# Kernel tuning notes

Measured on AMD Instinct MI355X. Metric: run time of the kernel, lower is better.

## Reference

```python
import jax, jax.numpy as jnp
import numpy as np

E = 1024   # embed_dim
H = 16     # num_heads
D = E // H # head_dim
T = 1024   # tgt_len
S = 1024   # src_len
B = 2      # batch
DELTA = 1.0
SCALE = D ** -0.5


def setup_inputs() -> dict:
    key = jax.random.key(0)
    ks = jax.random.split(key, 16)
    def lin(k, o, i):
        return jax.random.normal(k, (o, i), dtype=jnp.float32) / np.float32(np.sqrt(i))
    return {
        'query': jax.random.normal(ks[0], (T, B, E), dtype=jnp.float32),
        'key_in': jax.random.normal(ks[1], (S, B, E), dtype=jnp.float32),
        'value': jax.random.normal(ks[2], (S, B, E), dtype=jnp.float32),
        'Wq': lin(ks[3], E, E), 'bq': jnp.zeros((E,), jnp.float32),
        'Wk': lin(ks[4], E, E), 'bk': jnp.zeros((E,), jnp.float32),
        'Wv': lin(ks[5], E, E), 'bv': jnp.zeros((E,), jnp.float32),
        'Whq': lin(ks[6], E, E), 'bhq': jnp.zeros((E,), jnp.float32),
        'Whk': lin(ks[7], E, E), 'bhk': jnp.zeros((E,), jnp.float32),
        'Wwp': lin(ks[8], E, E), 'bwp': jnp.zeros((E,), jnp.float32),
        'Wvp': lin(ks[9], 1, E), 'bvp': jnp.zeros((1,), jnp.float32),
        'Wo': lin(ks[10], E, E), 'bo': jnp.zeros((E,), jnp.float32),
    }


def _heads(x, L):
    # (L, B, E) -> (B*H, L, D); E splits as (H, D) so flat index is b*H + h
    return x.reshape(L, B * H, D).transpose(1, 0, 2)


def reference(query, key_in, value, Wq, bq, Wk, bk, Wv, bv, Whq, bhq, Whk, bhk,
              Wwp, bwp, Wvp, bvp, Wo, bo):
    q = (query @ Wq.T + bq) * SCALE
    k = key_in @ Wk.T + bk
    v = value @ Wv.T + bv
    hq = query @ Whq.T + bhq
    hk = key_in @ Whk.T + bhk

    qh, hqh = _heads(q, T), _heads(hq, T)
    kh, hkh, vh = _heads(k, S), _heads(hk, S), _heads(v, S)

    # content attention logits  [B*H, T, S]
    attn = jnp.einsum('btd,bsd->bts', qh, kh)

    # Gaussian center: expected source position from hq/hk alignment
    align = jax.nn.softmax(jnp.einsum('btd,bsd->bts', hqh * SCALE, hkh), axis=-1)
    pos = jnp.arange(S, dtype=attn.dtype)          # index_mask
    mean = align @ pos                              # [B*H, T]

    # Gaussian width: per-query scalar via vp(tanh(wp(query)))
    g = (jnp.tanh(query @ Wwp.T + bwp) @ Wvp.T + bvp)[..., 0]   # (T, B)
    sigma = 1.0 + DELTA * jax.nn.sigmoid(g)                      # (T, B)
    sigma_bh = jnp.broadcast_to(sigma[:, :, None], (T, B, H)).reshape(T, B * H).T

    gauss = -((pos[None, None, :] - mean[:, :, None]) ** 2) / (
        2.0 * sigma_bh[:, :, None] ** 2)

    probs = jax.nn.softmax(attn + gauss, axis=-1)
    out = jnp.einsum('bts,bsd->btd', probs, vh)     # [B*H, T, D]
    out = out.transpose(1, 0, 2).reshape(T, B, E)
    return out @ Wo.T + bo
```

## Files before the change

### kernel.cpp

```cpp
#include <hip/hip_runtime.h>
#include <hip/hip_bf16.h>
#include <hip/hip_fp16.h>

#define T_ 1024
#define S_ 1024
#define B_ 2
#define H_ 16
#define D_ 64
#define E_ 1024
#define M_ (T_*B_)
#define SCALE_ 0.125f
#define LOG2E_ 1.4426950408889634f

typedef __attribute__((ext_vector_type(8))) short short8;
typedef __attribute__((ext_vector_type(8))) _Float16 half8;
typedef __attribute__((ext_vector_type(4))) float f32x4;

#define EXP2 __builtin_amdgcn_exp2f

__device__ __forceinline__ ushort f2bf(float x) {
  unsigned u = __float_as_uint(x);
  unsigned r = (u + 0x7fffu + ((u >> 16) & 1u)) >> 16;
  return (ushort)r;
}
__device__ __forceinline__ float bf2f(ushort h) {
  return __uint_as_float(((unsigned)h) << 16);
}
__device__ __forceinline__ ushort f2h(float x) {
  __half h = __float2half(x);
  return *(ushort*)&h;
}
__device__ __forceinline__ void gld16(const void* g, void* l) {
  __builtin_amdgcn_global_load_lds(
      (const __attribute__((address_space(1))) void*)g,
      (__attribute__((address_space(3))) void*)l, 16, 0, 0);
}
__device__ __forceinline__ unsigned cvtpk_bf16(float a, float b) {
  unsigned u;
  asm("v_cvt_pk_bf16_f32 %0, %1, %2" : "=v"(u) : "v"(a), "v"(b));
  return u;
}

#define SWZ(r, col) ((r)*64 + ((col) ^ (((r)&7)<<3)))

struct CvtDesc { const float* src; ushort* bf; ushort* h16; int n4; };
struct CvtArgs { CvtDesc d[10]; };

__global__ __launch_bounds__(256) void cvt_kernel(CvtArgs a) {
  const CvtDesc d = a.d[blockIdx.y];
  const int stride = gridDim.x * 256;
  for (int i = blockIdx.x*256 + threadIdx.x; i < d.n4; i += stride) {
    float4 v = ((const float4*)d.src)[i];
    float vals[4] = {v.x, v.y, v.z, v.w};
    if (d.bf) {
      ushort h[4];
      #pragma unroll
      for (int j = 0; j < 4; ++j) h[j] = f2bf(vals[j]);
      ((ushort4*)d.bf)[i] = make_ushort4(h[0],h[1],h[2],h[3]);
    }
    if (d.h16) {
      ushort h[4];
      #pragma unroll
      for (int j = 0; j < 4; ++j) h[j] = f2h(vals[j]);
      ((ushort4*)d.h16)[i] = make_ushort4(h[0],h[1],h[2],h[3]);
    }
  }
}

struct SegP { const ushort* A; const ushort* W; const float* bias;
              ushort* outb; float* outf; float scale; int flags; };
struct GemmArgs { SegP s[6]; };

__global__ __launch_bounds__(256) void gemm_mfma(GemmArgs args) {
  __shared__ ushort sA[128*64];
  __shared__ ushort sW[64*64];
  const int id = blockIdx.x;
  const int xcd = id & 7, loc = id >> 3;
  const int x = xcd * (gridDim.x >> 7) + (loc >> 4);
  const int y = loc & 15;
  const SegP sg = args.s[x >> 4];
  const int n0 = (x & 15) * 64;
  const int m0 = y * 128;
  const int tid = threadIdx.x, wv = tid >> 6, lane = tid & 63;
  const int c = lane & 15, g = lane >> 4;
  const int wr = wv >> 1, wc = wv & 1;
  const int lrow = lane >> 3;
  const int scol = ((lane & 7) ^ lrow) * 8;

  size_t aoff[4], woff[2];
  #pragma unroll
  for (int j = 0; j < 4; ++j) {
    int rg = wv + j*4;
    aoff[j] = (size_t)(m0 + rg*8 + lrow)*1024 + scol;
  }
  #pragma unroll
  for (int j = 0; j < 2; ++j) {
    int rg = wv + j*4;
    woff[j] = (size_t)(n0 + rg*8 + lrow)*1024 + scol;
  }

  const bool isfp16 = (sg.flags & 2) != 0;
  f32x4 acc[4][2] = {};
  for (int t = 0; t < 16; ++t) {
    const int k0 = t*64;
    #pragma unroll
    for (int j = 0; j < 4; ++j) {
      int rg = wv + j*4;
      gld16(sg.A + aoff[j] + k0, &sA[rg*512]);
    }
    #pragma unroll
    for (int j = 0; j < 2; ++j) {
      int rg = wv + j*4;
      gld16(sg.W + woff[j] + k0, &sW[rg*512]);
    }
    __syncthreads();
    #pragma unroll
    for (int ks = 0; ks < 2; ++ks) {
      short8 af[4], wf[2];
      #pragma unroll
      for (int mi = 0; mi < 4; ++mi)
        af[mi] = *(const short8*)&sA[SWZ(wr*64 + mi*16 + c, ks*32 + g*8)];
      #pragma unroll
      for (int ni = 0; ni < 2; ++ni)
        wf[ni] = *(const short8*)&sW[SWZ(wc*32 + ni*16 + c, ks*32 + g*8)];
      if (isfp16) {
        #pragma unroll
        for (int mi = 0; mi < 4; ++mi)
          #pragma unroll
          for (int ni = 0; ni < 2; ++ni)
            acc[mi][ni] = __builtin_amdgcn_mfma_f32_16x16x32_f16(
                *(half8*)&af[mi], *(half8*)&wf[ni], acc[mi][ni], 0, 0, 0);
      } else {
        #pragma unroll
        for (int mi = 0; mi < 4; ++mi)
          #pragma unroll
          for (int ni = 0; ni < 2; ++ni)
            acc[mi][ni] = __builtin_amdgcn_mfma_f32_16x16x32_bf16(
                af[mi], wf[ni], acc[mi][ni], 0, 0, 0);
      }
    }
    __syncthreads();
  }

  #pragma unroll
  for (int ni = 0; ni < 2; ++ni) {
    int col = n0 + wc*32 + ni*16 + c;
    float bias = sg.bias[col];
    #pragma unroll
    for (int mi = 0; mi < 4; ++mi) {
      #pragma unroll
      for (int r = 0; r < 4; ++r) {
        int row = m0 + wr*64 + mi*16 + 4*g + r;
        float val = (acc[mi][ni][r] + bias) * sg.scale;
        if (sg.flags & 1) val = tanhf(val);
        if (isfp16)       sg.outb[(size_t)row*1024 + col] = f2h(val);
        else if (sg.outf) sg.outf[(size_t)row*1024 + col] = val;
        else              sg.outb[(size_t)row*1024 + col] = f2bf(val);
      }
    }
  }
}

__global__ __launch_bounds__(64) void vp_sigma(const ushort* __restrict__ wp,
    const float* __restrict__ Wvp, const float* __restrict__ bvp,
    float* __restrict__ sigma) {
  const int m = blockIdx.x;
  const int lane = threadIdx.x;
  float acc = 0.f;
  #pragma unroll
  for (int it = 0; it < 2; ++it) {
    int e = lane*8 + it*512;
    short8 a = *(const short8*)&wp[(size_t)m*E_ + e];
    float4 w0 = *(const float4*)&Wvp[e];
    float4 w1 = *(const float4*)&Wvp[e+4];
    acc += bf2f((ushort)a[0])*w0.x + bf2f((ushort)a[1])*w0.y
         + bf2f((ushort)a[2])*w0.z + bf2f((ushort)a[3])*w0.w
         + bf2f((ushort)a[4])*w1.x + bf2f((ushort)a[5])*w1.y
         + bf2f((ushort)a[6])*w1.z + bf2f((ushort)a[7])*w1.w;
  }
  #pragma unroll
  for (int o = 32; o; o >>= 1) acc += __shfl_xor(acc, o);
  if (lane == 0) {
    float gg = acc + bvp[0];
    sigma[m] = 1.f + 1.f/(1.f + __expf(-gg));
  }
}

__global__ __launch_bounds__(256) void attn_mfma(
    const ushort* __restrict__ q_bf, const ushort* __restrict__ k_bf,
    const ushort* __restrict__ v_bf,
    const ushort* __restrict__ hq_h16, const ushort* __restrict__ hk_h16,
    const float* __restrict__ sigma, ushort* __restrict__ ctx) {
  __shared__ ushort sK[2][64*64];
  __shared__ ushort sV[2][64*64];
  __shared__ ushort sP[4*16*64];

  const int id = blockIdx.x;
  const int loc = id >> 3;
  const int bh = (id & 7) * 4 + (loc >> 4);
  const int b = bh >> 4, h = bh & 15;
  const int t0 = (loc & 15) * 64;
  const int tid = threadIdx.x;
  const int wv = tid >> 6, lane = tid & 63;
  const int c = lane & 15, g = lane >> 4;
  const int qbase = t0 + wv * 16;
  const size_t rowstr = (size_t)B_ * E_;
  const size_t qoff = ((size_t)(qbase + c) * B_ + b) * E_ + h * 64;

  short8 qf[2];
  half8  hqf[2];
  #pragma unroll
  for (int cs = 0; cs < 2; ++cs) {
    qf[cs]  = *(const short8*)&q_bf[qoff + cs*32 + g*8];
    hqf[cs] = *(const half8*)&hq_h16[qoff + cs*32 + g*8];
  }

  const int str0 = wv*16 + (lane >> 3);
  const int str1 = str0 + 8;
  const int chk0 = ((lane & 7) ^ (str0 & 7)) * 8;
  const int chk1 = ((lane & 7) ^ (str1 & 7)) * 8;
  const int ldsst = (wv*16) * 64;

  float den = 0.f, num = 0.f;
  {
    gld16(hk_h16 + ((size_t)str0 * B_ + b) * E_ + h*64 + chk0, &sK[0][ldsst]);
    gld16(hk_h16 + ((size_t)str1 * B_ + b) * E_ + h*64 + chk1, &sK[0][ldsst + 512]);
    __syncthreads();
    for (int t = 0; t < 16; ++t) {
      const ushort* kb = sK[t & 1];
      if (t < 15) {
        int s0n = (t+1) * 64;
        gld16(hk_h16 + ((size_t)(s0n + str0) * B_ + b) * E_ + h*64 + chk0,
              &sK[(t+1) & 1][ldsst]);
        gld16(hk_h16 + ((size_t)(s0n + str1) * B_ + b) * E_ + h*64 + chk1,
              &sK[(t+1) & 1][ldsst + 512]);
      }
      f32x4 acc[4] = {};
      __builtin_amdgcn_s_setprio(1);
      #pragma unroll
      for (int m = 0; m < 4; ++m)
        #pragma unroll
        for (int cs = 0; cs < 2; ++cs)
          acc[m] = __builtin_amdgcn_mfma_f32_16x16x32_f16(
              *(const half8*)&kb[SWZ(c + 16*m, cs*32 + g*8)], hqf[cs], acc[m], 0,0,0);
      __builtin_amdgcn_s_setprio(0);

      float fs = (float)(t*64 + 4*g);
      #pragma unroll
      for (int m = 0; m < 4; ++m)
        #pragma unroll
        for (int r = 0; r < 4; ++r) {
          float e = EXP2(acc[m][r]);
          den += e;
          num += e * (fs + (float)(16*m + r));
        }
      __syncthreads();
    }
  }
  den += __shfl_xor(den, 16); den += __shfl_xor(den, 32);
  num += __shfl_xor(num, 16); num += __shfl_xor(num, 32);
  const float meanq = num / den;
  const float sg = sigma[(size_t)(qbase + c) * B_ + b];
  const float fct = -LOG2E_ / (2.f * sg * sg);

  f32x4 accO[4] = {};
  float denq = 0.f;
  {
    gld16(k_bf + ((size_t)str0 * B_ + b) * E_ + h*64 + chk0, &sK[0][ldsst]);
    gld16(k_bf + ((size_t)str1 * B_ + b) * E_ + h*64 + chk1, &sK[0][ldsst + 512]);
    {
      int s2 = (tid & 31) * 2, d0 = (tid >> 5) * 8;
      size_t off0 = ((size_t)s2 * B_ + b) * E_ + h * 64 + d0;
      uint4 ra = *(const uint4*)&v_bf[off0];
      uint4 rb = *(const uint4*)&v_bf[off0 + rowstr];
      const ushort* pa = (const ushort*)&ra;
      const ushort* pb = (const ushort*)&rb;
      #pragma unroll
      for (int j = 0; j < 8; ++j)
        *(unsigned*)&sV[0][SWZ(d0 + j, s2)] = (unsigned)pa[j] | ((unsigned)pb[j] << 16);
    }
    __syncthreads();

    const int s2v = (tid & 31) * 2, d0v = (tid >> 5) * 8;
    for (int t = 0; t < 16; ++t) {
      const int cur = t & 1;
      const ushort* kb = sK[cur];
      const ushort* vb = sV[cur];
      uint4 ra, rb;
      if (t < 15) {
        int s0n = (t+1) * 64;
        gld16(k_bf + ((size_t)(s0n + str0) * B_ + b) * E_ + h*64 + chk0,
              &sK[cur^1][ldsst]);
        gld16(k_bf + ((size_t)(s0n + str1) * B_ + b) * E_ + h*64 + chk1,
              &sK[cur^1][ldsst + 512]);
        size_t off0 = ((size_t)(s0n + s2v) * B_ + b) * E_ + h * 64 + d0v;
        ra = *(const uint4*)&v_bf[off0];
        rb = *(const uint4*)&v_bf[off0 + rowstr];
      }

      f32x4 accL[4] = {};
      __builtin_amdgcn_s_setprio(1);
      #pragma unroll
      for (int m = 0; m < 4; ++m)
        #pragma unroll
        for (int cs = 0; cs < 2; ++cs)
          accL[m] = __builtin_amdgcn_mfma_f32_16x16x32_bf16(
              *(const short8*)&kb[SWZ(c + 16*m, cs*32 + g*8)], qf[cs], accL[m], 0,0,0);
      __builtin_amdgcn_s_setprio(0);

      float fs = (float)(t*64 + 4*g);
      float psum = 0.f;
      #pragma unroll
      for (int m = 0; m < 4; ++m) {
        float pr[4];
        #pragma unroll
        for (int r = 0; r < 4; ++r) {
          float dd = fs + (float)(16*m + r) - meanq;
          pr[r] = EXP2(accL[m][r] + fct * dd * dd);
          psum += pr[r];
        }
        uint2 uu;
        uu.x = cvtpk_bf16(pr[0], pr[1]);
        uu.y = cvtpk_bf16(pr[2], pr[3]);
        *(uint2*)&sP[wv*1024 + SWZ(c, 16*m + 4*g)] = uu;
      }
      denq += psum;

      __builtin_amdgcn_s_setprio(1);
      #pragma unroll
      for (int n = 0; n < 4; ++n)
        #pragma unroll
        for (int cs = 0; cs < 2; ++cs)
          accO[n] = __builtin_amdgcn_mfma_f32_16x16x32_bf16(
              *(const short8*)&sP[wv*1024 + SWZ(c, cs*32 + 8*g)],
              *(const short8*)&vb[SWZ(c + 16*n, cs*32 + 8*g)],
              accO[n], 0,0,0);
      __builtin_amdgcn_s_setprio(0);

      if (t < 15) {
        const ushort *pa = (const ushort*)&ra, *pb = (const ushort*)&rb;
        #pragma unroll
        for (int j = 0; j < 8; ++j)
          *(unsigned*)&sV[cur^1][SWZ(d0v + j, s2v)] = (unsigned)pa[j] | ((unsigned)pb[j] << 16);
      }
      __syncthreads();
    }
  }

  denq += __shfl_xor(denq, 16);
  denq += __shfl_xor(denq, 32);
  float dinv[4];
  #pragma unroll
  for (int r = 0; r < 4; ++r) dinv[r] = 1.f / __shfl(denq, 4*g + r);

  #pragma unroll
  for (int r = 0; r < 4; ++r) {
    size_t row = ((size_t)(qbase + 4*g + r) * B_ + b) * E_ + h * 64;
    #pragma unroll
    for (int n = 0; n < 4; ++n)
      ctx[row + 16*n + c] = f2bf(accO[n][r] * dinv[r]);
  }
}

extern "C" void kernel_launch(void* const* d_in, const int* in_sizes, int n_in,
                              void* d_out, int out_size, void* d_ws, size_t ws_size,
                              hipStream_t stream) {
  const float* query  = (const float*)d_in[0];
  const float* key_in = (const float*)d_in[1];
  const float* value  = (const float*)d_in[2];
  const float* Wq  = (const float*)d_in[3];  const float* bq  = (const float*)d_in[4];
  const float* Wk  = (const float*)d_in[5];  const float* bk  = (const float*)d_in[6];
  const float* Wv  = (const float*)d_in[7];  const float* bv  = (const float*)d_in[8];
  const float* Whq = (const float*)d_in[9];  const float* bhq = (const float*)d_in[10];
  const float* Whk = (const float*)d_in[11]; const float* bhk = (const float*)d_in[12];
  const float* Wwp = (const float*)d_in[13]; const float* bwp = (const float*)d_in[14];
  const float* Wvp = (const float*)d_in[15]; const float* bvp = (const float*)d_in[16];
  const float* Wo  = (const float*)d_in[17]; const float* bo  = (const float*)d_in[18];

  const size_t AU = (size_t)M_ * E_;
  const size_t WU = (size_t)E_ * E_;
  char* p = (char*)d_ws;
  float*  sig       = (float*)p;  p += 16384;
  ushort* query_bf  = (ushort*)p; p += AU*2;
  ushort* key_bf    = (ushort*)p; p += AU*2;
  ushort* value_bf  = (ushort*)p; p += AU*2;
  ushort* query_h16 = (ushort*)p; p += AU*2;
  ushort* key_h16   = (ushort*)p; p += AU*2;
  ushort* Whq_h16   = (ushort*)p; p += WU*2;
  ushort* Whk_h16   = (ushort*)p; p += WU*2;
  ushort* Wq_bf     = (ushort*)p; p += WU*2;
  ushort* Wk_bf     = (ushort*)p; p += WU*2;
  ushort* Wv_bf     = (ushort*)p; p += WU*2;
  ushort* Wwp_bf    = (ushort*)p; p += WU*2;
  ushort* Wo_bf     = (ushort*)p; p += WU*2;
  ushort* hq_h16    = (ushort*)p; p += AU*2;
  ushort* hk_h16    = (ushort*)p; p += AU*2;
  ushort* q_bf      = (ushort*)p; p += AU*2;
  ushort* k_bf      = (ushort*)p; p += AU*2;
  ushort* v_out     = (ushort*)p; p += AU*2;
  ushort* wp_bf     = (ushort*)p; p += AU*2;
  ushort* ctx_bf    = query_h16;

  {
    CvtArgs a{};
    a.d[0] = {query,  query_bf, query_h16, (int)(AU/4)};
    a.d[1] = {key_in, key_bf,   key_h16,   (int)(AU/4)};
    a.d[2] = {value,  value_bf, nullptr,   (int)(AU/4)};
    a.d[3] = {Whq,    nullptr,  Whq_h16,   (int)(WU/4)};
    a.d[4] = {Whk,    nullptr,  Whk_h16,   (int)(WU/4)};
    a.d[5] = {Wq,     Wq_bf,    nullptr,   (int)(WU/4)};
    a.d[6] = {Wk,     Wk_bf,    nullptr,   (int)(WU/4)};
    a.d[7] = {Wv,     Wv_bf,    nullptr,   (int)(WU/4)};
    a.d[8] = {Wwp,    Wwp_bf,   nullptr,   (int)(WU/4)};
    a.d[9] = {Wo,     Wo_bf,    nullptr,   (int)(WU/4)};
    cvt_kernel<<<dim3(128, 10), 256, 0, stream>>>(a);
  }
  {
    GemmArgs a{};
    a.s[0] = {query_bf,  Wq_bf,   bq,  q_bf,   nullptr, SCALE_*LOG2E_, 0};
    a.s[1] = {query_bf,  Wwp_bf,  bwp, wp_bf,  nullptr, 1.f,           1};
    a.s[2] = {key_bf,    Wk_bf,   bk,  k_bf,   nullptr, 1.f,           0};
    a.s[3] = {value_bf,  Wv_bf,   bv,  v_out,  nullptr, 1.f,           0};
    a.s[4] = {query_h16, Whq_h16, bhq, hq_h16, nullptr, SCALE_*LOG2E_, 2};
    a.s[5] = {key_h16,   Whk_h16, bhk, hk_h16, nullptr, 1.f,           2};
    gemm_mfma<<<dim3(1536), 256, 0, stream>>>(a);
  }
  vp_sigma<<<dim3(M_), dim3(64), 0, stream>>>(wp_bf, Wvp, bvp, sig);
  attn_mfma<<<dim3(512), 256, 0, stream>>>(
      q_bf, k_bf, v_out, hq_h16, hk_h16, sig, ctx_bf);
  {
    GemmArgs a{};
    a.s[0] = {ctx_bf, Wo_bf, bo, nullptr, (float*)d_out, 1.f, 0};
    gemm_mfma<<<dim3(256), 256, 0, stream>>>(a);
  }
}
```

Baseline: 119.7 us.

## Fuse vp projection and sigmoid into GEMM epilogue and attention; template GEMM M-tile

The tanh(wp) GEMM epilogue now dots its values with Wvp in registers, reduces across lanes and atomically adds the partial sums into a sigma buffer that the convert kernel zeroes first. This removes the separate vp_sigma launch and the bf16 wp intermediate write and read. The sigmoid is applied inside the attention kernel instead. The GEMM is templated on the M tile, and the output projection uses 64-row tiles with 512 blocks to fill more CUs. The cost is float atomics, which make the summation order nondeterministic.

```diff
diff --git a/kernel.cpp b/kernel.cpp
--- a/kernel.cpp
+++ b/kernel.cpp
@@ -44,9 +44,13 @@
 #define SWZ(r, col) ((r)*64 + ((col) ^ (((r)&7)<<3)))
 
 struct CvtDesc { const float* src; ushort* bf; ushort* h16; int n4; };
-struct CvtArgs { CvtDesc d[10]; };
+struct CvtArgs { CvtDesc d[10]; float* zero; int zn; };
 
 __global__ __launch_bounds__(256) void cvt_kernel(CvtArgs a) {
+  if (a.zero && blockIdx.y == 0) {
+    for (int i = blockIdx.x*256 + threadIdx.x; i < a.zn; i += gridDim.x*256)
+      a.zero[i] = 0.f;
+  }
   const CvtDesc d = a.d[blockIdx.y];
   const int stride = gridDim.x * 256;
   for (int i = blockIdx.x*256 + threadIdx.x; i < d.n4; i += stride) {
@@ -68,28 +72,32 @@
 }
 
 struct SegP { const ushort* A; const ushort* W; const float* bias;
-              ushort* outb; float* outf; float scale; int flags; };
+              ushort* outb; float* outf; const float* vp; float scale; int flags; };
 struct GemmArgs { SegP s[6]; };
 
+template<int MT>
 __global__ __launch_bounds__(256) void gemm_mfma(GemmArgs args) {
-  __shared__ ushort sA[128*64];
+  constexpr int AG = MT/32;
+  constexpr int MI = MT/32;
+  constexpr int NY = 2048/MT;
+  __shared__ ushort sA[MT*64];
   __shared__ ushort sW[64*64];
   const int id = blockIdx.x;
   const int xcd = id & 7, loc = id >> 3;
-  const int x = xcd * (gridDim.x >> 7) + (loc >> 4);
-  const int y = loc & 15;
+  const int x = xcd * ((gridDim.x >> 3) / NY) + loc / NY;
+  const int y = loc % NY;
   const SegP sg = args.s[x >> 4];
   const int n0 = (x & 15) * 64;
-  const int m0 = y * 128;
+  const int m0 = y * MT;
   const int tid = threadIdx.x, wv = tid >> 6, lane = tid & 63;
   const int c = lane & 15, g = lane >> 4;
   const int wr = wv >> 1, wc = wv & 1;
   const int lrow = lane >> 3;
   const int scol = ((lane & 7) ^ lrow) * 8;
 
-  size_t aoff[4], woff[2];
+  size_t aoff[AG], woff[2];
   #pragma unroll
-  for (int j = 0; j < 4; ++j) {
+  for (int j = 0; j < AG; ++j) {
     int rg = wv + j*4;
     aoff[j] = (size_t)(m0 + rg*8 + lrow)*1024 + scol;
   }
@@ -100,11 +108,11 @@
   }
 
   const bool isfp16 = (sg.flags & 2) != 0;
-  f32x4 acc[4][2] = {};
+  f32x4 acc[MI][2] = {};
   for (int t = 0; t < 16; ++t) {
     const int k0 = t*64;
     #pragma unroll
-    for (int j = 0; j < 4; ++j) {
+    for (int j = 0; j < AG; ++j) {
       int rg = wv + j*4;
       gld16(sg.A + aoff[j] + k0, &sA[rg*512]);
     }
@@ -116,23 +124,23 @@
     __syncthreads();
     #pragma unroll
     for (int ks = 0; ks < 2; ++ks) {
-      short8 af[4], wf[2];
-      #pragma unroll
-      for (int mi = 0; mi < 4; ++mi)
-        af[mi] = *(const short8*)&sA[SWZ(wr*64 + mi*16 + c, ks*32 + g*8)];
+      short8 af[MI], wf[2];
+      #pragma unroll
+      for (int mi = 0; mi < MI; ++mi)
+        af[mi] = *(const short8*)&sA[SWZ(wr*(MT/2) + mi*16 + c, ks*32 + g*8)];
       #pragma unroll
       for (int ni = 0; ni < 2; ++ni)
         wf[ni] = *(const short8*)&sW[SWZ(wc*32 + ni*16 + c, ks*32 + g*8)];
       if (isfp16) {
         #pragma unroll
-        for (int mi = 0; mi < 4; ++mi)
+        for (int mi = 0; mi < MI; ++mi)
           #pragma unroll
           for (int ni = 0; ni < 2; ++ni)
             acc[mi][ni] = __builtin_amdgcn_mfma_f32_16x16x32_f16(
                 *(half8*)&af[mi], *(half8*)&wf[ni], acc[mi][ni], 0, 0, 0);
       } else {
         #pragma unroll
-        for (int mi = 0; mi < 4; ++mi)
+        for (int mi = 0; mi < MI; ++mi)
           #pragma unroll
           for (int ni = 0; ni < 2; ++ni)
             acc[mi][ni] = __builtin_amdgcn_mfma_f32_16x16x32_bf16(
@@ -142,47 +150,44 @@
     __syncthreads();
   }
 
-  #pragma unroll
-  for (int ni = 0; ni < 2; ++ni) {
-    int col = n0 + wc*32 + ni*16 + c;
-    float bias = sg.bias[col];
-    #pragma unroll
-    for (int mi = 0; mi < 4; ++mi) {
+  if (sg.flags & 1) {
+    const int col0 = n0 + wc*32 + c, col1 = col0 + 16;
+    const float b0 = sg.bias[col0], b1 = sg.bias[col1];
+    const float w0 = sg.vp[col0],  w1 = sg.vp[col1];
+    #pragma unroll
+    for (int mi = 0; mi < MI; ++mi) {
       #pragma unroll
       for (int r = 0; r < 4; ++r) {
-        int row = m0 + wr*64 + mi*16 + 4*g + r;
-        float val = (acc[mi][ni][r] + bias) * sg.scale;
-        if (sg.flags & 1) val = tanhf(val);
-        if (isfp16)       sg.outb[(size_t)row*1024 + col] = f2h(val);
-        else if (sg.outf) sg.outf[(size_t)row*1024 + col] = val;
-        else              sg.outb[(size_t)row*1024 + col] = f2bf(val);
-      }
-    }
-  }
-}
-
-__global__ __launch_bounds__(64) void vp_sigma(const ushort* __restrict__ wp,
-    const float* __restrict__ Wvp, const float* __restrict__ bvp,
-    float* __restrict__ sigma) {
-  const int m = blockIdx.x;
-  const int lane = threadIdx.x;
-  float acc = 0.f;
-  #pragma unroll
-  for (int it = 0; it < 2; ++it) {
-    int e = lane*8 + it*512;
-    short8 a = *(const short8*)&wp[(size_t)m*E_ + e];
-    float4 w0 = *(const float4*)&Wvp[e];
-    float4 w1 = *(const float4*)&Wvp[e+4];
-    acc += bf2f((ushort)a[0])*w0.x + bf2f((ushort)a[1])*w0.y
-         + bf2f((ushort)a[2])*w0.z + bf2f((ushort)a[3])*w0.w
-         + bf2f((ushort)a[4])*w1.x + bf2f((ushort)a[5])*w1.y
-         + bf2f((ushort)a[6])*w1.z + bf2f((ushort)a[7])*w1.w;
-  }
-  #pragma unroll
-  for (int o = 32; o; o >>= 1) acc += __shfl_xor(acc, o);
-  if (lane == 0) {
-    float gg = acc + bvp[0];
-    sigma[m] = 1.f + 1.f/(1.f + __expf(-gg));
+        float v0 = tanhf((acc[mi][0][r] + b0) * sg.scale);
+        float v1 = tanhf((acc[mi][1][r] + b1) * sg.scale);
+        float part = v0*w0 + v1*w1;
+        part += __shfl_xor(part, 1);
+        part += __shfl_xor(part, 2);
+        part += __shfl_xor(part, 4);
+        part += __shfl_xor(part, 8);
+        if (c == 0) {
+          int row = m0 + wr*(MT/2) + mi*16 + 4*g + r;
+          atomicAdd(&sg.outf[row], part);
+        }
+      }
+    }
+  } else {
+    #pragma unroll
+    for (int ni = 0; ni < 2; ++ni) {
+      int col = n0 + wc*32 + ni*16 + c;
+      float bias = sg.bias[col];
+      #pragma unroll
+      for (int mi = 0; mi < MI; ++mi) {
+        #pragma unroll
+        for (int r = 0; r < 4; ++r) {
+          int row = m0 + wr*(MT/2) + mi*16 + 4*g + r;
+          float val = (acc[mi][ni][r] + bias) * sg.scale;
+          if (isfp16)       sg.outb[(size_t)row*1024 + col] = f2h(val);
+          else if (sg.outf) sg.outf[(size_t)row*1024 + col] = val;
+          else              sg.outb[(size_t)row*1024 + col] = f2bf(val);
+        }
+      }
+    }
   }
 }
 
@@ -190,7 +195,8 @@
     const ushort* __restrict__ q_bf, const ushort* __restrict__ k_bf,
     const ushort* __restrict__ v_bf,
     const ushort* __restrict__ hq_h16, const ushort* __restrict__ hk_h16,
-    const float* __restrict__ sigma, ushort* __restrict__ ctx) {
+    const float* __restrict__ sig_raw, const float* __restrict__ bvp,
+    ushort* __restrict__ ctx) {
   __shared__ ushort sK[2][64*64];
   __shared__ ushort sV[2][64*64];
   __shared__ ushort sP[4*16*64];
@@ -260,8 +266,9 @@
   den += __shfl_xor(den, 16); den += __shfl_xor(den, 32);
   num += __shfl_xor(num, 16); num += __shfl_xor(num, 32);
   const float meanq = num / den;
-  const float sg = sigma[(size_t)(qbase + c) * B_ + b];
-  const float fct = -LOG2E_ / (2.f * sg * sg);
+  const float graw = sig_raw[(size_t)(qbase + c) * B_ + b] + bvp[0];
+  const float sgm = 1.f + 1.f/(1.f + __expf(-graw));
+  const float fct = -LOG2E_ / (2.f * sgm * sgm);
 
   f32x4 accO[4] = {};
   float denq = 0.f;
@@ -398,7 +405,6 @@
   ushort* q_bf      = (ushort*)p; p += AU*2;
   ushort* k_bf      = (ushort*)p; p += AU*2;
   ushort* v_out     = (ushort*)p; p += AU*2;
-  ushort* wp_bf     = (ushort*)p; p += AU*2;
   ushort* ctx_bf    = query_h16;
 
   {
@@ -413,24 +419,24 @@
     a.d[7] = {Wv,     Wv_bf,    nullptr,   (int)(WU/4)};
     a.d[8] = {Wwp,    Wwp_bf,   nullptr,   (int)(WU/4)};
     a.d[9] = {Wo,     Wo_bf,    nullptr,   (int)(WU/4)};
+    a.zero = sig; a.zn = M_;
     cvt_kernel<<<dim3(128, 10), 256, 0, stream>>>(a);
   }
   {
     GemmArgs a{};
-    a.s[0] = {query_bf,  Wq_bf,   bq,  q_bf,   nullptr, SCALE_*LOG2E_, 0};
-    a.s[1] = {query_bf,  Wwp_bf,  bwp, wp_bf,  nullptr, 1.f,           1};
-    a.s[2] = {key_bf,    Wk_bf,   bk,  k_bf,   nullptr, 1.f,           0};
-    a.s[3] = {value_bf,  Wv_bf,   bv,  v_out,  nullptr, 1.f,           0};
-    a.s[4] = {query_h16, Whq_h16, bhq, hq_h16, nullptr, SCALE_*LOG2E_, 2};
-    a.s[5] = {key_h16,   Whk_h16, bhk, hk_h16, nullptr, 1.f,           2};
-    gemm_mfma<<<dim3(1536), 256, 0, stream>>>(a);
-  }
-  vp_sigma<<<dim3(M_), dim3(64), 0, stream>>>(wp_bf, Wvp, bvp, sig);
+    a.s[0] = {query_bf,  Wq_bf,   bq,  q_bf,   nullptr, nullptr, SCALE_*LOG2E_, 0};
+    a.s[1] = {query_bf,  Wwp_bf,  bwp, nullptr, sig,    Wvp,     1.f,           1};
+    a.s[2] = {key_bf,    Wk_bf,   bk,  k_bf,   nullptr, nullptr, 1.f,           0};
+    a.s[3] = {value_bf,  Wv_bf,   bv,  v_out,  nullptr, nullptr, 1.f,           0};
+    a.s[4] = {query_h16, Whq_h16, bhq, hq_h16, nullptr, nullptr, SCALE_*LOG2E_, 2};
+    a.s[5] = {key_h16,   Whk_h16, bhk, hk_h16, nullptr, nullptr, 1.f,           2};
+    gemm_mfma<128><<<dim3(1536), 256, 0, stream>>>(a);
+  }
   attn_mfma<<<dim3(512), 256, 0, stream>>>(
-      q_bf, k_bf, v_out, hq_h16, hk_h16, sig, ctx_bf);
+      q_bf, k_bf, v_out, hq_h16, hk_h16, sig, bvp, ctx_bf);
   {
     GemmArgs a{};
-    a.s[0] = {ctx_bf, Wo_bf, bo, nullptr, (float*)d_out, 1.f, 0};
-    gemm_mfma<<<dim3(256), 256, 0, stream>>>(a);
-  }
-}
+    a.s[0] = {ctx_bf, Wo_bf, bo, nullptr, (float*)d_out, nullptr, 1.f, 0};
+    gemm_mfma<64><<<dim3(512), 256, 0, stream>>>(a);
+  }
+}
```

New measurement: 112.3 us (median of 2 runs). -6.2%, faster.
